# Performance work log

Hardware: AMD Instinct MI355X
Metric: run time of the kernel (lower is better)

The kernel has to match this reference:

```python
import jax, jax.numpy as jnp
import numpy as np

D_MODEL = 1024
NH_KD = 1024
RANK = 16
ALPHA = 1.0
SCALING = ALPHA / RANK


def setup_inputs() -> dict:
    key = jax.random.key(0)
    ks = jax.random.split(key, 7)
    std = 1.0 / np.sqrt(D_MODEL)
    x = jax.random.normal(ks[0], (4, 4096, D_MODEL), dtype=jnp.float32)
    # torch nn.Linear weight layout: [out, in]
    w_qkv = jax.random.normal(ks[1], (3 * NH_KD, D_MODEL), dtype=jnp.float32) * std
    b_qkv = jax.random.normal(ks[2], (3 * NH_KD,), dtype=jnp.float32) * 0.01
    a_q = jax.random.normal(ks[3], (RANK, D_MODEL), dtype=jnp.float32) * std
    b_q = jnp.zeros((NH_KD, RANK), dtype=jnp.float32) + jax.random.normal(ks[4], (NH_KD, RANK), dtype=jnp.float32) * 0.02
    a_v = jax.random.normal(ks[5], (RANK, D_MODEL), dtype=jnp.float32) * std
    b_v = jnp.zeros((NH_KD, RANK), dtype=jnp.float32) + jax.random.normal(ks[6], (NH_KD, RANK), dtype=jnp.float32) * 0.02
    return {"x": x, "w_qkv": w_qkv, "b_qkv": b_qkv, "a_q": a_q, "b_q": b_q, "a_v": a_v, "b_v": b_v}


def reference(x, w_qkv, b_qkv, a_q, b_q, a_v, b_v):
    # base QKV: [B,S,D] x [3*nh_kd, D]^T -> [B,S,3*nh_kd]
    qkv = jnp.einsum('bsd,od->bso', x, w_qkv) + b_qkv
    q = qkv[..., :NH_KD]
    k = qkv[..., NH_KD:2 * NH_KD]
    v = qkv[..., 2 * NH_KD:]
    # LoRA: x @ a^T @ b^T, scaled
    q = q + jnp.einsum('bsr,or->bso', jnp.einsum('bsd,rd->bsr', x, a_q), b_q) * SCALING
    v = v + jnp.einsum('bsr,or->bso', jnp.einsum('bsd,rd->bsr', x, a_v), b_v) * SCALING
    return jnp.concatenate([q, k, v], axis=-1)
```

## Files before the change

kernel.cpp:

```cpp
#include <hip/hip_runtime.h>

typedef unsigned int u32;
typedef unsigned short u16;
typedef short s16x8 __attribute__((ext_vector_type(8)));
typedef u16 u16x8 __attribute__((ext_vector_type(8)));
typedef float f32x4 __attribute__((ext_vector_type(4)));
typedef __attribute__((address_space(3))) u32 as3_u32;
typedef __attribute__((address_space(1))) const u32 as1_u32;

constexpr int MM = 16384, NN = 3072, KK = 1024;
constexpr int BM = 256, BN = 256, BK = 64;
constexpr int NT = KK / BK;

template <int V> struct IC { static constexpr int value = V; };

__device__ __forceinline__ u16 f2bf(float f) {
  u32 u = __builtin_bit_cast(u32, f);
  u = (u + 0x7FFFu + ((u >> 16) & 1u)) >> 16;
  return (u16)u;
}

__device__ __forceinline__ void gload_lds16(const void* g, void* l) {
  __builtin_amdgcn_global_load_lds((as1_u32*)g, (as3_u32*)l, 16, 0, 0);
}

constexpr int WEFF_BLOCKS = NN * KK / 256;
constexpr int CVT_BLOCKS = MM * KK / 8 / 256;
__global__ __launch_bounds__(256) void prep(
    const float* __restrict__ w, const float* __restrict__ aq,
    const float* __restrict__ bq, const float* __restrict__ av,
    const float* __restrict__ bv, u16* __restrict__ weff,
    const float* __restrict__ x, u16* __restrict__ xb) {
  const int bid = blockIdx.x;
  if (bid < WEFF_BLOCKS) {
    int idx = bid * 256 + threadIdx.x;
    int o = idx >> 10, d = idx & 1023;
    float val = w[idx];
    if (o < 1024) {
      float s = 0.f;
#pragma unroll
      for (int r = 0; r < 16; ++r) s += bq[o * 16 + r] * aq[r * 1024 + d];
      val += s * 0.0625f;
    } else if (o >= 2048) {
      int o2 = o - 2048;
      float s = 0.f;
#pragma unroll
      for (int r = 0; r < 16; ++r) s += bv[o2 * 16 + r] * av[r * 1024 + d];
      val += s * 0.0625f;
    }
    weff[idx] = f2bf(val);
  } else {
    size_t i = ((size_t)(bid - WEFF_BLOCKS) * 256 + threadIdx.x) * 8;
    float4 f0 = *(const float4*)(x + i);
    float4 f1 = *(const float4*)(x + i + 4);
    u16x8 o;
    o[0] = f2bf(f0.x); o[1] = f2bf(f0.y); o[2] = f2bf(f0.z); o[3] = f2bf(f0.w);
    o[4] = f2bf(f1.x); o[5] = f2bf(f1.y); o[6] = f2bf(f1.z); o[7] = f2bf(f1.w);
    *(u16x8*)(xb + i) = o;
  }
}

__global__ __launch_bounds__(512, 2) void gemm8p(
    const u16* __restrict__ Ag, const u16* __restrict__ Bg,
    const float* __restrict__ bias, float* __restrict__ C) {
  __shared__ __align__(16) u16 sA[2][BM * BK];
  __shared__ __align__(16) u16 sB[2][BN * BK];

  const int tid = threadIdx.x;
  const int wave = tid >> 6, lane = tid & 63;
  const int wrow = wave >> 2, wcol = wave & 3;
  const int l15 = lane & 15, lk = lane >> 4;
  const int swz = (l15 & 7) << 4;
  const int ko0 = ((lk * 16) ^ swz) >> 1;
  const int ko1 = ((64 + lk * 16) ^ swz) >> 1;
  const int sRow = lane >> 3;
  const int sCol = ((lane & 7) ^ (lane >> 3)) << 3;

  constexpr int NWG = (MM / BM) * (NN / BN);
  const int b = blockIdx.x;
  const int bs = (b & 7) * (NWG >> 3) + (b >> 3);
  const int tileM = (bs / (NN / BN)) * BM;
  const int tileN = (bs % (NN / BN)) * BN;

  const u16* Agb = Ag + (size_t)tileM * KK;
  const u16* Bgb = Bg + (size_t)tileN * KK;

  f32x4 acc[8][4] = {};
  s16x8 a[4][2], bl[2][2], bh[2][2];

  auto STAGE = [&](const u16* __restrict__ G, int rowHalf, u16* ldsHalf, int kc) {
#pragma unroll
    for (int j = 0; j < 2; ++j) {
      const int c = wave * 2 + j;
      gload_lds16(G + (size_t)(rowHalf + c * 8 + sRow) * KK + kc + sCol,
                  ldsHalf + c * 512);
    }
  };
  auto LDA = [&](const u16* At, int mh) {
#pragma unroll
    for (int i = 0; i < 4; ++i) {
      const int row = wrow * 128 + (mh * 4 + i) * 16 + l15;
      const u16* p = At + row * 64;
      a[i][0] = *(const s16x8*)(p + ko0);
      a[i][1] = *(const s16x8*)(p + ko1);
    }
  };
  auto LDB = [&](s16x8 (&bf)[2][2], const u16* Bt, int nh) {
#pragma unroll
    for (int i = 0; i < 2; ++i) {
      const int row = wcol * 64 + (nh * 2 + i) * 16 + l15;
      const u16* p = Bt + row * 64;
      bf[i][0] = *(const s16x8*)(p + ko0);
      bf[i][1] = *(const s16x8*)(p + ko1);
    }
  };
  auto MFMA16 = [&](auto MH, auto NH, s16x8 (&bf)[2][2]) {
    constexpr int mh = decltype(MH)::value, nh = decltype(NH)::value;
    __builtin_amdgcn_s_setprio(1);
#pragma unroll
    for (int k2 = 0; k2 < 2; ++k2)
#pragma unroll
      for (int i = 0; i < 4; ++i)
#pragma unroll
        for (int j = 0; j < 2; ++j)
          acc[mh * 4 + i][nh * 2 + j] = __builtin_amdgcn_mfma_f32_16x16x32_bf16(
              a[i][k2], bf[j][k2], acc[mh * 4 + i][nh * 2 + j], 0, 0, 0);
    __builtin_amdgcn_s_setprio(0);
  };
  auto BAR = [] {
    asm volatile("" ::: "memory");
    __builtin_amdgcn_s_barrier();
    asm volatile("" ::: "memory");
  };

  auto KT = [&](int cb, int k1, int k2, int s1, int s2, int vm) {
    const u16* Ac = sA[cb]; const u16* Bc = sB[cb];
    LDA(Ac, 0); LDB(bl, Bc, 0);
    if (s1) STAGE(Agb, 0, sA[cb ^ 1], k1);
    BAR();
    MFMA16(IC<0>{}, IC<0>{}, bl);
    LDB(bh, Bc, 1);
    if (s1) STAGE(Agb, 128, sA[cb ^ 1] + 8192, k1);
    asm volatile("s_waitcnt lgkmcnt(0)" ::: "memory");
    BAR();
    MFMA16(IC<0>{}, IC<1>{}, bh);
    LDA(Ac, 1);
    if (s2) STAGE(Bgb, 0, sB[cb], k2);
    BAR();
    MFMA16(IC<1>{}, IC<1>{}, bh);
    if (s2) STAGE(Bgb, 128, sB[cb] + 8192, k2);
    MFMA16(IC<1>{}, IC<0>{}, bl);
    if (vm == 4) asm volatile("s_waitcnt vmcnt(4)" ::: "memory");
    else if (vm == 0) asm volatile("s_waitcnt vmcnt(0)" ::: "memory");
    BAR();
  };

  STAGE(Agb, 0,   sA[0], 0);
  STAGE(Agb, 128, sA[0] + 8192, 0);
  STAGE(Bgb, 0,   sB[0], 0);
  STAGE(Bgb, 128, sB[0] + 8192, 0);
  STAGE(Bgb, 0,   sB[1], BK);
  STAGE(Bgb, 128, sB[1] + 8192, BK);
  asm volatile("s_waitcnt vmcnt(4)" ::: "memory");
  BAR();

#pragma unroll 1
  for (int t = 0; t < NT - 2; t += 2) {
    KT(0, (t + 1) * BK, (t + 2) * BK, 1, 1, 4);
    KT(1, (t + 2) * BK, (t + 3) * BK, 1, 1, 4);
  }
  KT(0, (NT - 1) * BK, 0, 1, 0, 0);
  KT(1, 0, 0, 0, 0, -1);

  const int r0 = tileM + wrow * 128, c0 = tileN + wcol * 64;
#pragma unroll
  for (int n = 0; n < 4; ++n) {
    const int col = c0 + n * 16 + l15;
    const float bv = bias[col];
#pragma unroll
    for (int m = 0; m < 8; ++m) {
      const int rr = r0 + m * 16 + lk * 4;
#pragma unroll
      for (int j = 0; j < 4; ++j)
        C[(size_t)(rr + j) * NN + col] = acc[m][n][j] + bv;
    }
  }
}

__global__ __launch_bounds__(256) void gemm_fb(
    const float* __restrict__ Af, const u16* __restrict__ Bw,
    const float* __restrict__ bias, float* __restrict__ C) {
  __shared__ u16 As[128 * 64];
  __shared__ u16 Bs[128 * 64];
  const int tid = threadIdx.x;
  const int wave = tid >> 6, lane = tid & 63;
  const int l15 = lane & 15, lkq = lane >> 4;
  const int mTile = blockIdx.y * 128, nTile = blockIdx.x * 128;
  const int wr = wave >> 1, wc = wave & 1;
  f32x4 acc[4][4] = {};
  for (int k0 = 0; k0 < KK; k0 += 64) {
#pragma unroll
    for (int j = 0; j < 4; ++j) {
      const int c = wave * 4 + j;
      const int e = c * 512 + lane * 8;
      const int row = e >> 6, col = e & 63;
      gload_lds16(Bw + (size_t)(nTile + row) * KK + k0 + col, Bs + c * 512);
    }
#pragma unroll
    for (int j = 0; j < 4; ++j) {
      const int e = (j * 256 + tid) * 8;
      const int row = e >> 6, col = e & 63;
      const float* g = Af + (size_t)(mTile + row) * KK + k0 + col;
      float4 f0 = *(const float4*)g;
      float4 f1 = *(const float4*)(g + 4);
      u16x8 o;
      o[0] = f2bf(f0.x); o[1] = f2bf(f0.y); o[2] = f2bf(f0.z); o[3] = f2bf(f0.w);
      o[4] = f2bf(f1.x); o[5] = f2bf(f1.y); o[6] = f2bf(f1.z); o[7] = f2bf(f1.w);
      *(u16x8*)(As + e) = o;
    }
    __syncthreads();
    s16x8 af[4][2], bf[4][2];
#pragma unroll
    for (int m = 0; m < 4; ++m)
#pragma unroll
      for (int t = 0; t < 2; ++t)
        af[m][t] = *(const s16x8*)(As + (wr * 64 + m * 16 + l15) * 64 + t * 32 + lkq * 8);
#pragma unroll
    for (int n = 0; n < 4; ++n)
#pragma unroll
      for (int t = 0; t < 2; ++t)
        bf[n][t] = *(const s16x8*)(Bs + (wc * 64 + n * 16 + l15) * 64 + t * 32 + lkq * 8);
#pragma unroll
    for (int t = 0; t < 2; ++t)
#pragma unroll
      for (int m = 0; m < 4; ++m)
#pragma unroll
        for (int n = 0; n < 4; ++n)
          acc[m][n] = __builtin_amdgcn_mfma_f32_16x16x32_bf16(af[m][t], bf[n][t],
                                                              acc[m][n], 0, 0, 0);
    __syncthreads();
  }
  const int row0 = mTile + wr * 64, col0 = nTile + wc * 64;
#pragma unroll
  for (int n = 0; n < 4; ++n) {
    const int col = col0 + n * 16 + l15;
    const float bv = bias[col];
#pragma unroll
    for (int m = 0; m < 4; ++m) {
      const int rr = row0 + m * 16 + lkq * 4;
#pragma unroll
      for (int j = 0; j < 4; ++j)
        C[(size_t)(rr + j) * NN + col] = acc[m][n][j] + bv;
    }
  }
}

extern "C" void kernel_launch(void* const* d_in, const int* in_sizes, int n_in,
                              void* d_out, int out_size, void* d_ws, size_t ws_size,
                              hipStream_t stream) {
  const float* x     = (const float*)d_in[0];
  const float* w_qkv = (const float*)d_in[1];
  const float* b_qkv = (const float*)d_in[2];
  const float* a_q   = (const float*)d_in[3];
  const float* b_q   = (const float*)d_in[4];
  const float* a_v   = (const float*)d_in[5];
  const float* b_v   = (const float*)d_in[6];
  float* out = (float*)d_out;

  u16* weff = (u16*)d_ws;
  const size_t weff_elems = (size_t)NN * KK;
  u16* xb = weff + weff_elems;
  const size_t need = (weff_elems + (size_t)MM * KK) * sizeof(u16);

  if (ws_size >= need) {
    prep<<<dim3(WEFF_BLOCKS + CVT_BLOCKS), dim3(256), 0, stream>>>(
        w_qkv, a_q, b_q, a_v, b_v, weff, x, xb);
    gemm8p<<<dim3((MM / BM) * (NN / BN)), dim3(512), 0, stream>>>(xb, weff,
                                                                  b_qkv, out);
  } else {
    prep<<<dim3(WEFF_BLOCKS), dim3(256), 0, stream>>>(w_qkv, a_q, b_q, a_v,
                                                      b_v, weff, x, nullptr);
    gemm_fb<<<dim3(NN / 128, MM / 128), dim3(256), 0, stream>>>(x, weff,
                                                                b_qkv, out);
  }
}
```

Baseline: 149.8 us.

## Double-buffer A fragments and prefetch next tile's registers across barriers

Splits the A register fragments into two sets so the next K-tile's first A and B fragments can be loaded from LDS at the end of the current iteration. The schedule of LDS reads, global-to-LDS staging, vmcnt waits and barriers inside the K loop is reordered to overlap register loads with MFMA work, and the prologue staging order changes. This costs extra VGPRs and more barriers per iteration, which may lower occupancy or add sync stalls, and the finer wait counts must match the number of outstanding loads.

```diff
diff --git a/kernel.cpp b/kernel.cpp
--- a/kernel.cpp
+++ b/kernel.cpp
@@ -86,7 +86,7 @@
   const u16* Bgb = Bg + (size_t)tileN * KK;
 
   f32x4 acc[8][4] = {};
-  s16x8 a[4][2], bl[2][2], bh[2][2];
+  s16x8 a0[4][2], a1[4][2], bl[2][2], bh[2][2];
 
   auto STAGE = [&](const u16* __restrict__ G, int rowHalf, u16* ldsHalf, int kc) {
 #pragma unroll
@@ -96,13 +96,13 @@
                   ldsHalf + c * 512);
     }
   };
-  auto LDA = [&](const u16* At, int mh) {
+  auto LDA = [&](s16x8 (&af)[4][2], const u16* At, int mh) {
 #pragma unroll
     for (int i = 0; i < 4; ++i) {
       const int row = wrow * 128 + (mh * 4 + i) * 16 + l15;
       const u16* p = At + row * 64;
-      a[i][0] = *(const s16x8*)(p + ko0);
-      a[i][1] = *(const s16x8*)(p + ko1);
+      af[i][0] = *(const s16x8*)(p + ko0);
+      af[i][1] = *(const s16x8*)(p + ko1);
     }
   };
   auto LDB = [&](s16x8 (&bf)[2][2], const u16* Bt, int nh) {
@@ -114,7 +114,7 @@
       bf[i][1] = *(const s16x8*)(p + ko1);
     }
   };
-  auto MFMA16 = [&](auto MH, auto NH, s16x8 (&bf)[2][2]) {
+  auto MFMA16 = [&](s16x8 (&af)[4][2], s16x8 (&bf)[2][2], auto MH, auto NH) {
     constexpr int mh = decltype(MH)::value, nh = decltype(NH)::value;
     __builtin_amdgcn_s_setprio(1);
 #pragma unroll
@@ -124,7 +124,7 @@
 #pragma unroll
         for (int j = 0; j < 2; ++j)
           acc[mh * 4 + i][nh * 2 + j] = __builtin_amdgcn_mfma_f32_16x16x32_bf16(
-              a[i][k2], bf[j][k2], acc[mh * 4 + i][nh * 2 + j], 0, 0, 0);
+              af[i][k2], bf[j][k2], acc[mh * 4 + i][nh * 2 + j], 0, 0, 0);
     __builtin_amdgcn_s_setprio(0);
   };
   auto BAR = [] {
@@ -132,45 +132,61 @@
     __builtin_amdgcn_s_barrier();
     asm volatile("" ::: "memory");
   };
-
-  auto KT = [&](int cb, int k1, int k2, int s1, int s2, int vm) {
-    const u16* Ac = sA[cb]; const u16* Bc = sB[cb];
-    LDA(Ac, 0); LDB(bl, Bc, 0);
+  auto VMG = [](int n) {
+    if (n == 6) asm volatile("s_waitcnt vmcnt(6)" ::: "memory");
+    else if (n == 4) asm volatile("s_waitcnt vmcnt(4)" ::: "memory");
+    else if (n == 2) asm volatile("s_waitcnt vmcnt(2)" ::: "memory");
+    else if (n == 0) asm volatile("s_waitcnt vmcnt(0)" ::: "memory");
+  };
+
+  auto KT = [&](int cb, int k1, int k2, int s1, int s2, int g1, int g2, int ra) {
+    LDB(bh, sB[cb], 1);
     if (s1) STAGE(Agb, 0, sA[cb ^ 1], k1);
     BAR();
-    MFMA16(IC<0>{}, IC<0>{}, bl);
-    LDB(bh, Bc, 1);
+    asm volatile("s_waitcnt lgkmcnt(4)" ::: "memory");
+    MFMA16(a0, bl, IC<0>{}, IC<0>{});
+    VMG(g1);
+    BAR();
+    LDA(a1, sA[cb], 1);
     if (s1) STAGE(Agb, 128, sA[cb ^ 1] + 8192, k1);
+    BAR();
+    asm volatile("s_waitcnt lgkmcnt(8)" ::: "memory");
+    MFMA16(a0, bh, IC<0>{}, IC<1>{});
+    BAR();
+    if (s2) STAGE(Bgb, 0, sB[cb], k2);
+    BAR();
     asm volatile("s_waitcnt lgkmcnt(0)" ::: "memory");
-    BAR();
-    MFMA16(IC<0>{}, IC<1>{}, bh);
-    LDA(Ac, 1);
-    if (s2) STAGE(Bgb, 0, sB[cb], k2);
-    BAR();
-    MFMA16(IC<1>{}, IC<1>{}, bh);
+    MFMA16(a1, bh, IC<1>{}, IC<1>{});
+    VMG(g2);
+    BAR();
     if (s2) STAGE(Bgb, 128, sB[cb] + 8192, k2);
-    MFMA16(IC<1>{}, IC<0>{}, bl);
-    if (vm == 4) asm volatile("s_waitcnt vmcnt(4)" ::: "memory");
-    else if (vm == 0) asm volatile("s_waitcnt vmcnt(0)" ::: "memory");
-    BAR();
-  };
-
+    MFMA16(a1, bl, IC<1>{}, IC<0>{});
+    if (ra) {
+      LDA(a0, sA[cb ^ 1], 0);
+      LDB(bl, sB[cb ^ 1], 0);
+    }
+    BAR();
+  };
+
+  STAGE(Bgb, 0,   sB[0], 0);
+  STAGE(Bgb, 128, sB[0] + 8192, 0);
   STAGE(Agb, 0,   sA[0], 0);
   STAGE(Agb, 128, sA[0] + 8192, 0);
-  STAGE(Bgb, 0,   sB[0], 0);
-  STAGE(Bgb, 128, sB[0] + 8192, 0);
   STAGE(Bgb, 0,   sB[1], BK);
   STAGE(Bgb, 128, sB[1] + 8192, BK);
   asm volatile("s_waitcnt vmcnt(4)" ::: "memory");
   BAR();
+  LDA(a0, sA[0], 0);
+  LDB(bl, sB[0], 0);
+  BAR();
 
 #pragma unroll 1
   for (int t = 0; t < NT - 2; t += 2) {
-    KT(0, (t + 1) * BK, (t + 2) * BK, 1, 1, 4);
-    KT(1, (t + 2) * BK, (t + 3) * BK, 1, 1, 4);
-  }
-  KT(0, (NT - 1) * BK, 0, 1, 0, 0);
-  KT(1, 0, 0, 0, 0, -1);
+    KT(0, (t + 1) * BK, (t + 2) * BK, 1, 1, 6, 4, 1);
+    KT(1, (t + 2) * BK, (t + 3) * BK, 1, 1, 6, 4, 1);
+  }
+  KT(0, (NT - 1) * BK, 0, 1, 0, 6, 2, 1);
+  KT(1, 0, 0, 0, 0, 0, -1, 0);
 
   const int r0 = tileM + wrow * 128, c0 = tileN + wcol * 64;
 #pragma unroll
```

Result: slower. 274.4 us (+83.2%).

## Load B operand directly from global into registers, drop B LDS staging

Applied to the files above, without the earlier changes.

The GEMM no longer stages the weight tile in LDS. Each wave loads its B fragments straight from global memory into double-buffered registers (even and odd k-tiles), while A is still staged into LDS via global_load_lds. The block-to-tile mapping also changes so that groups of M tiles share an N column for L2 reuse. This halves LDS use and removes the LDS reads for B. In exchange it adds register pressure and duplicates B global loads across the two wave rows, which may stall on L2 latency.

```diff
diff --git a/kernel.cpp b/kernel.cpp
--- a/kernel.cpp
+++ b/kernel.cpp
@@ -60,11 +60,10 @@
   }
 }
 
-__global__ __launch_bounds__(512, 2) void gemm8p(
+__global__ __launch_bounds__(512, 2) void gemm_bd(
     const u16* __restrict__ Ag, const u16* __restrict__ Bg,
     const float* __restrict__ bias, float* __restrict__ C) {
   __shared__ __align__(16) u16 sA[2][BM * BK];
-  __shared__ __align__(16) u16 sB[2][BN * BK];
 
   const int tid = threadIdx.x;
   const int wave = tid >> 6, lane = tid & 63;
@@ -76,45 +75,42 @@
   const int sRow = lane >> 3;
   const int sCol = ((lane & 7) ^ (lane >> 3)) << 3;
 
-  constexpr int NWG = (MM / BM) * (NN / BN);
   const int b = blockIdx.x;
-  const int bs = (b & 7) * (NWG >> 3) + (b >> 3);
-  const int tileM = (bs / (NN / BN)) * BM;
-  const int tileN = (bs % (NN / BN)) * BN;
+  const int x = b & 7, c = b >> 3;
+  const int tileM = (x * 8 + (c & 7)) * BM;
+  const int tileN = (c >> 3) * BN;
 
   const u16* Agb = Ag + (size_t)tileM * KK;
-  const u16* Bgb = Bg + (size_t)tileN * KK;
+  const u16* Bb = Bg + (size_t)(tileN + wcol * 64 + l15) * KK + lk * 8;
 
   f32x4 acc[8][4] = {};
-  s16x8 a[4][2], bl[2][2], bh[2][2];
-
-  auto STAGE = [&](const u16* __restrict__ G, int rowHalf, u16* ldsHalf, int kc) {
-#pragma unroll
-    for (int j = 0; j < 2; ++j) {
-      const int c = wave * 2 + j;
-      gload_lds16(G + (size_t)(rowHalf + c * 8 + sRow) * KK + kc + sCol,
-                  ldsHalf + c * 512);
-    }
-  };
-  auto LDA = [&](const u16* At, int mh) {
+  s16x8 a[4][2], bE[4][2], bO[4][2];
+
+  auto STAGE_A = [&](int cb, int kc) {
+#pragma unroll
+    for (int j = 0; j < 4; ++j) {
+      const int ch = wave * 4 + j;
+      gload_lds16(Agb + (size_t)(ch * 8 + sRow) * KK + kc + sCol,
+                  sA[cb] + ch * 512);
+    }
+  };
+  auto LDBG = [&](s16x8 (&dst)[4][2], int kc) {
+#pragma unroll
+    for (int fn = 0; fn < 4; ++fn)
+#pragma unroll
+      for (int k2 = 0; k2 < 2; ++k2)
+        dst[fn][k2] = *(const s16x8*)(Bb + (size_t)fn * 16 * KK + kc + k2 * 32);
+  };
+  auto LDA = [&](int cb, int mh) {
 #pragma unroll
     for (int i = 0; i < 4; ++i) {
       const int row = wrow * 128 + (mh * 4 + i) * 16 + l15;
-      const u16* p = At + row * 64;
+      const u16* p = sA[cb] + row * 64;
       a[i][0] = *(const s16x8*)(p + ko0);
       a[i][1] = *(const s16x8*)(p + ko1);
     }
   };
-  auto LDB = [&](s16x8 (&bf)[2][2], const u16* Bt, int nh) {
-#pragma unroll
-    for (int i = 0; i < 2; ++i) {
-      const int row = wcol * 64 + (nh * 2 + i) * 16 + l15;
-      const u16* p = Bt + row * 64;
-      bf[i][0] = *(const s16x8*)(p + ko0);
-      bf[i][1] = *(const s16x8*)(p + ko1);
-    }
-  };
-  auto MFMA16 = [&](auto MH, auto NH, s16x8 (&bf)[2][2]) {
+  auto MFMA16 = [&](s16x8 (&bf)[4][2], auto MH, auto NH) {
     constexpr int mh = decltype(MH)::value, nh = decltype(NH)::value;
     __builtin_amdgcn_s_setprio(1);
 #pragma unroll
@@ -124,7 +120,7 @@
 #pragma unroll
         for (int j = 0; j < 2; ++j)
           acc[mh * 4 + i][nh * 2 + j] = __builtin_amdgcn_mfma_f32_16x16x32_bf16(
-              a[i][k2], bf[j][k2], acc[mh * 4 + i][nh * 2 + j], 0, 0, 0);
+              a[i][k2], bf[nh * 2 + j][k2], acc[mh * 4 + i][nh * 2 + j], 0, 0, 0);
     __builtin_amdgcn_s_setprio(0);
   };
   auto BAR = [] {
@@ -133,44 +129,40 @@
     asm volatile("" ::: "memory");
   };
 
-  auto KT = [&](int cb, int k1, int k2, int s1, int s2, int vm) {
-    const u16* Ac = sA[cb]; const u16* Bc = sB[cb];
-    LDA(Ac, 0); LDB(bl, Bc, 0);
-    if (s1) STAGE(Agb, 0, sA[cb ^ 1], k1);
-    BAR();
-    MFMA16(IC<0>{}, IC<0>{}, bl);
-    LDB(bh, Bc, 1);
-    if (s1) STAGE(Agb, 128, sA[cb ^ 1] + 8192, k1);
+  auto TILE = [&](int cb, s16x8 (&bcur)[4][2], int kc2, int iss, int gate) {
+    LDA(cb, 0);
+    BAR();
+    MFMA16(bcur, IC<0>{}, IC<0>{});
+    MFMA16(bcur, IC<0>{}, IC<1>{});
+    BAR();
+    LDA(cb, 1);
     asm volatile("s_waitcnt lgkmcnt(0)" ::: "memory");
     BAR();
-    MFMA16(IC<0>{}, IC<1>{}, bh);
-    LDA(Ac, 1);
-    if (s2) STAGE(Bgb, 0, sB[cb], k2);
-    BAR();
-    MFMA16(IC<1>{}, IC<1>{}, bh);
-    if (s2) STAGE(Bgb, 128, sB[cb] + 8192, k2);
-    MFMA16(IC<1>{}, IC<0>{}, bl);
-    if (vm == 4) asm volatile("s_waitcnt vmcnt(4)" ::: "memory");
-    else if (vm == 0) asm volatile("s_waitcnt vmcnt(0)" ::: "memory");
-    BAR();
-  };
-
-  STAGE(Agb, 0,   sA[0], 0);
-  STAGE(Agb, 128, sA[0] + 8192, 0);
-  STAGE(Bgb, 0,   sB[0], 0);
-  STAGE(Bgb, 128, sB[0] + 8192, 0);
-  STAGE(Bgb, 0,   sB[1], BK);
-  STAGE(Bgb, 128, sB[1] + 8192, BK);
-  asm volatile("s_waitcnt vmcnt(4)" ::: "memory");
+    MFMA16(bcur, IC<1>{}, IC<1>{});
+    MFMA16(bcur, IC<1>{}, IC<0>{});
+    if (iss) {
+      LDBG(bcur, kc2);
+      STAGE_A(cb, kc2);
+    }
+    if (gate == 12) asm volatile("s_waitcnt vmcnt(12)" ::: "memory");
+    else if (gate == 0) asm volatile("s_waitcnt vmcnt(0)" ::: "memory");
+    BAR();
+  };
+
+  LDBG(bE, 0);
+  STAGE_A(0, 0);
+  LDBG(bO, BK);
+  STAGE_A(1, BK);
+  asm volatile("s_waitcnt vmcnt(12)" ::: "memory");
   BAR();
 
 #pragma unroll 1
   for (int t = 0; t < NT - 2; t += 2) {
-    KT(0, (t + 1) * BK, (t + 2) * BK, 1, 1, 4);
-    KT(1, (t + 2) * BK, (t + 3) * BK, 1, 1, 4);
-  }
-  KT(0, (NT - 1) * BK, 0, 1, 0, 0);
-  KT(1, 0, 0, 0, 0, -1);
+    TILE(0, bE, (t + 2) * BK, 1, 12);
+    TILE(1, bO, (t + 3) * BK, 1, 12);
+  }
+  TILE(0, bE, 0, 0, 0);
+  TILE(1, bO, 0, 0, -1);
 
   const int r0 = tileM + wrow * 128, c0 = tileN + wcol * 64;
 #pragma unroll
@@ -201,10 +193,10 @@
   for (int k0 = 0; k0 < KK; k0 += 64) {
 #pragma unroll
     for (int j = 0; j < 4; ++j) {
-      const int c = wave * 4 + j;
-      const int e = c * 512 + lane * 8;
+      const int ch = wave * 4 + j;
+      const int e = ch * 512 + lane * 8;
       const int row = e >> 6, col = e & 63;
-      gload_lds16(Bw + (size_t)(nTile + row) * KK + k0 + col, Bs + c * 512);
+      gload_lds16(Bw + (size_t)(nTile + row) * KK + k0 + col, Bs + ch * 512);
     }
 #pragma unroll
     for (int j = 0; j < 4; ++j) {
@@ -275,8 +267,8 @@
   if (ws_size >= need) {
     prep<<<dim3(WEFF_BLOCKS + CVT_BLOCKS), dim3(256), 0, stream>>>(
         w_qkv, a_q, b_q, a_v, b_v, weff, x, xb);
-    gemm8p<<<dim3((MM / BM) * (NN / BN)), dim3(512), 0, stream>>>(xb, weff,
-                                                                  b_qkv, out);
+    gemm_bd<<<dim3((MM / BM) * (NN / BN)), dim3(512), 0, stream>>>(xb, weff,
+                                                                   b_qkv, out);
   } else {
     prep<<<dim3(WEFF_BLOCKS), dim3(256), 0, stream>>>(w_qkv, a_q, b_q, a_v,
                                                       b_v, weff, x, nullptr);
```

Result: slower. 220.3 us (+47.1%).
